# Kernel optimization log

Hardware: AMD Instinct MI355X
Metric: run time of the kernel (lower is better)

The kernel has to match this reference:

```python
import jax, jax.numpy as jnp
import numpy as np

B, S, E = 4, 2048, 1024
H = 4
DH = E // H          # 256 head dim
DQ = E // 4          # 256 quaternion d_model
ALPHA = 1.5
EPS = 1e-10
FOCUS = 0.9
SEL = 2.0


def setup_inputs() -> dict:
    key = jax.random.key(0)
    ks = jax.random.split(key, 6)
    sc = 0.02
    return {
        "x": jax.random.normal(ks[0], (B, S, E), dtype=jnp.float32),
        "in_proj_w": jax.random.normal(ks[1], (3 * E, E), dtype=jnp.float32) * sc,
        "in_proj_b": jnp.zeros((3 * E,), dtype=jnp.float32),
        "out_w": jax.random.normal(ks[2], (E, E), dtype=jnp.float32) * sc,
        "out_b": jnp.zeros((E,), dtype=jnp.float32),
        "m_w1": jax.random.normal(ks[3], (E, E), dtype=jnp.float32) * sc,
        "m_b1": jnp.zeros((E,), dtype=jnp.float32),
        "m_w2": jax.random.normal(ks[4], (E, E), dtype=jnp.float32) * sc,
        "m_b2": jnp.zeros((E,), dtype=jnp.float32),
    }


def quaternion_multiply(q1, q2):
    # Hamilton product over last dim of size 4 (complex-valued components).
    w1, x1, y1, z1 = q1[..., 0], q1[..., 1], q1[..., 2], q1[..., 3]
    w2, x2, y2, z2 = q2[..., 0], q2[..., 1], q2[..., 2], q2[..., 3]
    return jnp.stack([
        w1 * w2 - x1 * x2 - y1 * y2 - z1 * z2,
        w1 * x2 + x1 * w2 + y1 * z2 - z1 * y2,
        w1 * y2 - x1 * z2 + y1 * w2 + z1 * x2,
        w1 * z2 + x1 * y2 - y1 * x2 + z1 * w2,
    ], axis=-1)


def _mha(x, in_proj_w, in_proj_b, out_w, out_b):
    # torch nn.MultiheadAttention self-attention, batch_first
    qkv = x @ in_proj_w.T + in_proj_b              # [B,S,3E]
    q, k, v = jnp.split(qkv, 3, axis=-1)
    q = q.reshape(B, S, H, DH)
    k = k.reshape(B, S, H, DH)
    v = v.reshape(B, S, H, DH)
    scores = jnp.einsum('bqhd,bkhd->bhqk', q, k) / jnp.sqrt(jnp.float32(DH))
    attn = jax.nn.softmax(scores, axis=-1)
    out = jnp.einsum('bhqk,bkhd->bqhd', attn, v).reshape(B, S, E)
    return out @ out_w.T + out_b


def _spectral_attention(signal):
    sq = signal.reshape(B, S, DQ, 4)
    sfft = jnp.fft.fft(sq, axis=-3)                 # complex64, FFT over seq
    kk = jnp.arange(S, dtype=jnp.float32)
    filt = jnp.exp(1j * ALPHA * jnp.arctan(jnp.log(kk + EPS)))  # [S] complex
    sf = sfft * filt[None, :, None, None]
    inter = quaternion_multiply(quaternion_multiply(sf, sf), sf)
    attended = jnp.fft.ifft(inter, axis=-3).real
    return attended.reshape(B, S, E)


def reference(x, in_proj_w, in_proj_b, out_w, out_b, m_w1, m_b1, m_w2, m_b2):
    nicotinic = _mha(x, in_proj_w, in_proj_b, out_w, out_b)
    h = jax.nn.gelu(x @ m_w1.T + m_b1, approximate=False)
    muscarinic = h @ m_w2.T + m_b2
    chol = FOCUS * nicotinic + (1.0 - FOCUS) * muscarinic
    attn_w = _spectral_attention(chol * SEL)
    return x * attn_w
```

## Files before the change

### kernel.cpp

```cpp
#include <hip/hip_runtime.h>
#include <cstdint>

typedef _Float16 f16;
typedef unsigned short u16;
typedef __attribute__((ext_vector_type(8))) _Float16 half8;
typedef __attribute__((ext_vector_type(4))) _Float16 half4;
typedef __attribute__((ext_vector_type(2))) __fp16 fp16x2;
typedef __attribute__((ext_vector_type(4))) float f32x4;

#define MFMA_F16(a, b, c) __builtin_amdgcn_mfma_f32_16x16x32_f16(a, b, c, 0, 0, 0)

#define WAITVM8() asm volatile("s_waitcnt vmcnt(8)" ::: "memory")
#define WAITVM4() asm volatile("s_waitcnt vmcnt(4)" ::: "memory")
#define WAITVM2() asm volatile("s_waitcnt vmcnt(2)" ::: "memory")
#define WAITVM0() asm volatile("s_waitcnt vmcnt(0)" ::: "memory")
#define BARRIER() do { asm volatile("" ::: "memory"); __builtin_amdgcn_s_barrier(); \
                       asm volatile("" ::: "memory"); } while (0)

__device__ inline void stage16(const void* g, void* l) {
#if defined(__has_builtin) && __has_builtin(__builtin_amdgcn_global_load_lds)
  __builtin_amdgcn_global_load_lds(
      (const __attribute__((address_space(1))) unsigned*)g,
      (__attribute__((address_space(3))) unsigned*)l, 16, 0, 0);
#else
  *(int4*)l = *(const int4*)g;
#endif
}

__device__ inline int pack_f16(float a, float b) {
#if defined(__has_builtin) && __has_builtin(__builtin_amdgcn_cvt_pkrtz)
  union { fp16x2 h; int i; } u;
  u.h = __builtin_amdgcn_cvt_pkrtz(a, b);
  return u.i;
#else
  union { f16 h[2]; int i; } u;
  u.h[0] = (f16)a; u.h[1] = (f16)b;
  return u.i;
#endif
}

__global__ __launch_bounds__(256)
void conv_all(const float* __restrict__ x, const float* __restrict__ wqkv,
              const float* __restrict__ w1, const float* __restrict__ wout,
              const float* __restrict__ w2, f16* __restrict__ dst) {
  int i = (blockIdx.x * 256 + threadIdx.x) * 8;
  const float* src; size_t dofs; float sc = 1.0f;
  if (i < 8388608)       { src = x + i;               dofs = i; }
  else if (i < 11534336) { src = wqkv + (i - 8388608); dofs = i; }
  else if (i < 12582912) { src = w1 + (i - 11534336);  dofs = i; }
  else if (i < 13631488) {
    int t = i - 12582912; int j = t >> 10, k = t & 1023;
    src = wout + t; dofs = 12582912 + (size_t)j * 2048 + k; sc = 1.8f;
  } else {
    int t = i - 13631488; int j = t >> 10, k = t & 1023;
    src = w2 + t; dofs = 12582912 + (size_t)j * 2048 + 1024 + k; sc = 0.2f;
  }
  float4 a = *(const float4*)src;
  float4 b = *(const float4*)(src + 4);
  half8 h;
  h[0] = (f16)(a.x * sc); h[1] = (f16)(a.y * sc); h[2] = (f16)(a.z * sc); h[3] = (f16)(a.w * sc);
  h[4] = (f16)(b.x * sc); h[5] = (f16)(b.y * sc); h[6] = (f16)(b.z * sc); h[7] = (f16)(b.w * sc);
  *(half8*)(dst + dofs) = h;
}

template<int EPI>
__global__ __launch_bounds__(256, 2)
void gemm_f16(const f16* __restrict__ A, const f16* __restrict__ W,
              const float* __restrict__ bias0, const float* __restrict__ bias1,
              void* __restrict__ out0, void* __restrict__ out1,
              f16* __restrict__ Vt, int N, int K) {
  __shared__ __align__(16) f16 lds[2][16384];
  const int tid = threadIdx.x;
  const int lane = tid & 63, w = tid >> 6;
  const int g = lane >> 4, lm = lane & 15;
  const int wr = w >> 1, wc = w & 1;
  const int nwg = gridDim.x * gridDim.y;
  const int flat = blockIdx.y * gridDim.x + blockIdx.x;
  const int logical = (flat & 7) * (nwg >> 3) + (flat >> 3);
  const int bx = logical % gridDim.x, by = logical / gridDim.x;
  const int m0 = by * 128, n0 = bx * 128;

  const f16* src[8];
#pragma unroll
  for (int j = 0; j < 8; ++j) {
    int u = j * 256 + tid;
    if (u < 1024) {
      int row = u >> 3, s = u & 7;
      src[j] = A + (size_t)(m0 + row) * K + ((s ^ (row & 7)) << 3);
    } else {
      int v = u - 1024;
      int row = v >> 3, s = v & 7;
      src[j] = W + (size_t)(n0 + row) * K + ((s ^ (row & 7)) << 3);
    }
  }

  f32x4 acc[4][4];
#pragma unroll
  for (int mt = 0; mt < 4; ++mt)
#pragma unroll
    for (int nt = 0; nt < 4; ++nt) acc[mt][nt] = (f32x4){0.f, 0.f, 0.f, 0.f};

#pragma unroll
  for (int j = 0; j < 8; ++j) stage16(src[j], &lds[0][(j * 256 + tid) * 8]);
  __syncthreads();

  const int KT = K >> 6;
#pragma unroll 1
  for (int t = 0; t < KT; ++t) {
    const f16* bufA = lds[t & 1];
    const f16* bufB = bufA + 8192;
    if (t + 1 < KT) {
#pragma unroll
      for (int j = 0; j < 8; ++j) {
        src[j] += 64;
        stage16(src[j], &lds[(t + 1) & 1][(j * 256 + tid) * 8]);
      }
      WAITVM8();
    } else {
      WAITVM0();
    }
    BARRIER();
#pragma unroll
    for (int ks = 0; ks < 2; ++ks) {
      half8 a[4], b[4];
#pragma unroll
      for (int mt = 0; mt < 4; ++mt) {
        int row = wr * 64 + mt * 16 + lm;
        a[mt] = *(const half8*)(bufA + row * 64 + (((ks * 4 + g) ^ (row & 7)) << 3));
      }
#pragma unroll
      for (int nt = 0; nt < 4; ++nt) {
        int row = wc * 64 + nt * 16 + lm;
        b[nt] = *(const half8*)(bufB + row * 64 + (((ks * 4 + g) ^ (row & 7)) << 3));
      }
#pragma unroll
      for (int mt = 0; mt < 4; ++mt)
#pragma unroll
        for (int nt = 0; nt < 4; ++nt)
          acc[mt][nt] = MFMA_F16(a[mt], b[nt], acc[mt][nt]);
    }
    BARRIER();
  }

  const int crow = m0 + wr * 64 + g * 4;
  const int ccol = n0 + wc * 64 + lm;
  if (EPI == 3) {
    if (n0 < 2048) {
      f16* qk = (f16*)out0;
#pragma unroll
      for (int nt = 0; nt < 4; ++nt) {
        float bb = bias0[ccol + nt * 16];
#pragma unroll
        for (int mt = 0; mt < 4; ++mt)
#pragma unroll
          for (int r = 0; r < 4; ++r)
            qk[(size_t)(crow + mt * 16 + r) * 3072 + ccol + nt * 16] =
                (f16)(acc[mt][nt][r] + bb);
      }
    } else if (n0 < 3072) {
      f16* ldsT = (f16*)lds;
#pragma unroll
      for (int nt = 0; nt < 4; ++nt) {
        float bb = bias0[ccol + nt * 16];
        int c = wc * 64 + nt * 16 + lm;
#pragma unroll
        for (int mt = 0; mt < 4; ++mt) {
          int r = wr * 64 + mt * 16 + g * 4;
#pragma unroll
          for (int rr = 0; rr < 4; ++rr)
            ldsT[c * 136 + r + rr] = (f16)(acc[mt][nt][rr] + bb);
        }
      }
      BARRIER();
      const int vbase0 = n0 - 2048;
      const int b = m0 >> 11, srow = m0 & 2047;
#pragma unroll
      for (int it = 0; it < 8; ++it) {
        int id = it * 256 + tid;
        int c = id >> 4, rb = id & 15;
        int vcol = vbase0 + c;
        int h = vcol >> 8, d = vcol & 255;
        half8 v = *(half8*)&ldsT[c * 136 + rb * 8];
        *(half8*)&Vt[(((size_t)(b * 4 + h)) * 256 + d) * 2048 + srow + rb * 8] = v;
      }
    } else {
      f16* cat = (f16*)out1;
      const int hc = ccol - 3072;
#pragma unroll
      for (int nt = 0; nt < 4; ++nt) {
        float bb = bias1[hc + nt * 16];
#pragma unroll
        for (int mt = 0; mt < 4; ++mt)
#pragma unroll
          for (int r = 0; r < 4; ++r) {
            float v = acc[mt][nt][r] + bb;
            v = 0.5f * v * (1.0f + erff(v * 0.70710678118654752f));
            cat[(size_t)(crow + mt * 16 + r) * 2048 + 1024 + hc + nt * 16] = (f16)v;
          }
      }
    }
  } else {
    f16* ch = (f16*)out0;
#pragma unroll
    for (int nt = 0; nt < 4; ++nt) {
      float bb = 1.8f * bias0[ccol + nt * 16] + 0.2f * bias1[ccol + nt * 16];
#pragma unroll
      for (int mt = 0; mt < 4; ++mt)
#pragma unroll
        for (int r = 0; r < 4; ++r)
          ch[(size_t)(crow + mt * 16 + r) * 1024 + ccol + nt * 16] =
              (f16)(acc[mt][nt][r] + bb);
    }
  }
}

__global__ __launch_bounds__(512, 2)
void flash_f16(const f16* __restrict__ qkv, const f16* __restrict__ Vt,
               f16* __restrict__ attn) {
  __shared__ __align__(16) f16 lds[32768];
  const int tid = threadIdx.x;
  const int lane = tid & 63, w = tid >> 6;
  const int g = lane >> 4, lm = lane & 15;
  const int raw = blockIdx.x;
  const int bh = (raw & 7) * 2 + (raw >> 7);
  const int qt = (raw >> 3) & 15;
  const int b = bh >> 2, h = bh & 3;
  const int q0 = qt * 128 + w * 16;
  const float SC = 0.09016844005555896f;

  half8 qf[8];
  {
    const f16* qp = qkv + (size_t)(b * 2048 + q0 + lm) * 3072 + h * 256 + g * 8;
#pragma unroll
    for (int c = 0; c < 8; ++c) qf[c] = *(const half8*)(qp + c * 32);
  }

  const f16* kbase = qkv + (size_t)b * 2048 * 3072 + 1024 + h * 256;
  const f16* vbase = Vt + (size_t)bh * 256 * 2048;
  int kofs[2], vofs[2];
#pragma unroll
  for (int j = 0; j < 2; ++j) {
    int u = j * 512 + tid;
    int kv = u >> 5, s = u & 31;
    kofs[j] = kv * 3072 + ((s ^ (kv & 7)) << 3);
    int d = u >> 2, sl = u & 3;
    vofs[j] = d * 2048 + ((sl ^ ((d >> 1) & 3)) << 3);
  }

  f32x4 o[16];
#pragma unroll
  for (int f = 0; f < 16; ++f) o[f] = (f32x4){0.f, 0.f, 0.f, 0.f};
  float m = -3e38f, l = 0.f;
  half8 paP = (half8){0, 0, 0, 0, 0, 0, 0, 0};

#pragma unroll
  for (int j = 0; j < 2; ++j) stage16(kbase + kofs[j], &lds[(j * 512 + tid) * 8]);

#pragma unroll 1
  for (int t = 0; t < 64; ++t) {
    const int cb_ = t & 1;
    if (t < 63) {
      const int kt = (t + 1) * 98304;
#pragma unroll
      for (int j = 0; j < 2; ++j)
        stage16(kbase + kofs[j] + kt, &lds[(cb_ ^ 1) * 8192 + (j * 512 + tid) * 8]);
    }
    {
      const int vt_ = t * 32;
#pragma unroll
      for (int j = 0; j < 2; ++j)
        stage16(vbase + vofs[j] + vt_, &lds[16384 + cb_ * 8192 + (j * 512 + tid) * 8]);
    }
    if (t < 63) { WAITVM4(); } else { WAITVM2(); }
    BARRIER();

    const f16* kb = &lds[cb_ * 8192];

    f32x4 s0 = {0.f, 0.f, 0.f, 0.f}, s1 = {0.f, 0.f, 0.f, 0.f};
    __builtin_amdgcn_s_setprio(1);
#pragma unroll
    for (int c = 0; c < 8; ++c) {
      int slot = ((c * 4 + g) ^ (lm & 7)) << 3;
      half8 b0 = *(const half8*)(kb + lm * 256 + slot);
      half8 b1 = *(const half8*)(kb + (16 + lm) * 256 + slot);
      s0 = MFMA_F16(b0, qf[c], s0);
      s1 = MFMA_F16(b1, qf[c], s1);
    }
    __builtin_amdgcn_s_setprio(0);

    if (t > 0) {
      const f16* vbp = &lds[16384 + (cb_ ^ 1) * 8192];
      __builtin_amdgcn_s_setprio(1);
#pragma unroll
      for (int f = 0; f < 16; ++f) {
        int d = f * 16 + lm;
        half8 bv = *(const half8*)(vbp + d * 32 + ((g ^ ((d >> 1) & 3)) << 3));
        o[f] = MFMA_F16(paP, bv, o[f]);
      }
      __builtin_amdgcn_s_setprio(0);
    }

    float a0[4], a1[4];
#pragma unroll
    for (int r = 0; r < 4; ++r) { a0[r] = s0[r] * SC; a1[r] = s1[r] * SC; }
    float mx = fmaxf(fmaxf(fmaxf(a0[0], a0[1]), fmaxf(a0[2], a0[3])),
                     fmaxf(fmaxf(a1[0], a1[1]), fmaxf(a1[2], a1[3])));
    mx = fmaxf(mx, __shfl_xor(mx, 16));
    mx = fmaxf(mx, __shfl_xor(mx, 32));

    if (!__all(mx <= m + 8.0f)) {
      float mn = fmaxf(m, mx);
      float corr = exp2f(m - mn);
      m = mn; l *= corr;
#pragma unroll
      for (int r = 0; r < 4; ++r) {
        float cr = __shfl(corr, ((lane >> 2) & 12) + r);
#pragma unroll
        for (int f = 0; f < 16; ++f) o[f][r] *= cr;
      }
    }

    float e0[4], e1[4], rs;
#pragma unroll
    for (int r = 0; r < 4; ++r) { e0[r] = exp2f(a0[r] - m); e1[r] = exp2f(a1[r] - m); }
    rs = ((e0[0] + e0[1]) + (e0[2] + e0[3])) + ((e1[0] + e1[1]) + (e1[2] + e1[3]));
    rs += __shfl_xor(rs, 16);
    rs += __shfl_xor(rs, 32);
    l += rs;

    int A01 = pack_f16(e0[0], e0[1]);
    int A23 = pack_f16(e0[2], e0[3]);
    int B01 = pack_f16(e1[0], e1[1]);
    int B23 = pack_f16(e1[2], e1[3]);
    const int s1l = ((lane & 16) << 1) + lm;
    const int s2l = s1l + 16;
    int t0a = __shfl(A01, s1l), t0b = __shfl(B01, s1l);
    int t1a = __shfl(A23, s1l), t1b = __shfl(B23, s1l);
    int t2a = __shfl(A01, s2l), t2b = __shfl(B01, s2l);
    int t3a = __shfl(A23, s2l), t3b = __shfl(B23, s2l);
    union { int i[4]; half8 h; } pau;
    const bool hi = lane >= 32;
    pau.i[0] = hi ? t0b : t0a;
    pau.i[1] = hi ? t1b : t1a;
    pau.i[2] = hi ? t2b : t2a;
    pau.i[3] = hi ? t3b : t3a;
    paP = pau.h;

    BARRIER();
  }

  WAITVM0();
  BARRIER();
  {
    const f16* vbp = &lds[16384 + 8192];
#pragma unroll
    for (int f = 0; f < 16; ++f) {
      int d = f * 16 + lm;
      half8 bv = *(const half8*)(vbp + d * 32 + ((g ^ ((d >> 1) & 3)) << 3));
      o[f] = MFMA_F16(paP, bv, o[f]);
    }
  }

  float inv[4];
#pragma unroll
  for (int r = 0; r < 4; ++r) inv[r] = 1.0f / __shfl(l, ((lane >> 2) & 12) + r);
#pragma unroll
  for (int f = 0; f < 16; ++f)
#pragma unroll
    for (int r = 0; r < 4; ++r)
      attn[(size_t)(b * 2048 + q0 + g * 4 + r) * 2048 + h * 256 + f * 16 + lm] =
          (f16)(o[f][r] * inv[r]);
}

__device__ inline float2 cmul(float2 a, float2 b) {
  return make_float2(a.x * b.x - a.y * b.y, a.x * b.y + a.y * b.x);
}
__device__ inline float2 cmulc(float2 a, float2 b) {
  return make_float2(a.x * b.x + a.y * b.y, a.y * b.x - a.x * b.y);
}
__device__ inline void qcube(float2& w, float2& x, float2& y, float2& z, float2 f) {
  w = cmul(w, f); x = cmul(x, f); y = cmul(y, f); z = cmul(z, f);
  float2 a2 = cmul(w, w);
  float2 sx = cmul(x, x), sy = cmul(y, y), sz = cmul(z, z);
  float2 s = make_float2(sx.x + sy.x + sz.x, sx.y + sy.y + sz.y);
  float2 t3 = make_float2(a2.x - 3.f * s.x, a2.y - 3.f * s.y);
  float2 cf = make_float2(3.f * a2.x - s.x, 3.f * a2.y - s.y);
  w = cmul(w, t3); x = cmul(cf, x); y = cmul(cf, y); z = cmul(cf, z);
}

__device__ inline int fftpos(int k) {
  int kp = k >> 1;
  return ((k & 1) << 10) | ((kp & 3) << 8) | ((kp & 12) << 4) | (kp & 48)
       | ((kp >> 4) & 12) | ((kp >> 8) & 3);
}

__global__ __launch_bounds__(256)
void spectral4(const f16* __restrict__ chol, const float* __restrict__ xin,
               float* __restrict__ outp) {
  __shared__ __align__(16) float2 Z[2][2048];
  __shared__ float2 tw[1024];
  const int tid = threadIdx.x;
  const int b = blockIdx.x >> 8;
  const int qd = blockIdx.x & 255;
  const size_t c0 = (size_t)qd * 4;
  const f16* cb = chol + (size_t)b * 2048 * 1024;

  for (int j = tid; j < 1024; j += 256) {
    float ang = -6.2831853071795864769f * (float)j * (1.0f / 2048.0f);
    float sv, cv; sincosf(ang, &sv, &cv);
    tw[j] = make_float2(cv, sv);
  }
  for (int s = tid; s < 2048; s += 256) {
    half4 v = *(const half4*)(cb + (size_t)s * 1024 + c0);
    Z[0][s] = make_float2((float)v[0], (float)v[1]);
    Z[1][s] = make_float2((float)v[2], (float)v[3]);
  }
  __syncthreads();

#pragma unroll 1
  for (int it = 0; it < 8; ++it) {
    int gg = it * 256 + tid;
    int c = gg >> 10, j = gg & 1023;
    float2 a = Z[c][j], bb = Z[c][j + 1024];
    Z[c][j] = make_float2(a.x + bb.x, a.y + bb.y);
    Z[c][j + 1024] = cmul(make_float2(a.x - bb.x, a.y - bb.y), tw[j]);
  }
  __syncthreads();

#pragma unroll 1
  for (int lq = 8; lq >= 0; lq -= 2) {
    const int Q = 1 << lq, st = 512 >> lq;
#pragma unroll 1
    for (int it = 0; it < 4; ++it) {
      int gg = it * 256 + tid;
      int c = gg >> 9, bf = gg & 511;
      int j = bf & (Q - 1);
      int base = ((bf >> lq) << (lq + 2)) | j;
      float2 a = Z[c][base], bq = Z[c][base + Q];
      float2 cc = Z[c][base + 2 * Q], d = Z[c][base + 3 * Q];
      float2 t0 = make_float2(a.x + cc.x, a.y + cc.y);
      float2 t1 = make_float2(a.x - cc.x, a.y - cc.y);
      float2 t2 = make_float2(bq.x + d.x, bq.y + d.y);
      float2 bd = make_float2(bq.x - d.x, bq.y - d.y);
      float2 t3 = make_float2(bd.y, -bd.x);
      float2 y0 = make_float2(t0.x + t2.x, t0.y + t2.y);
      float2 y1 = make_float2(t1.x + t3.x, t1.y + t3.y);
      float2 y2 = make_float2(t0.x - t2.x, t0.y - t2.y);
      float2 y3 = make_float2(t1.x - t3.x, t1.y - t3.y);
      int i3 = 3 * j * st;
      float sg = (i3 & 1024) ? -1.f : 1.f;
      i3 &= 1023;
      Z[c][base] = y0;
      Z[c][base + Q] = cmul(y1, tw[j * st]);
      Z[c][base + 2 * Q] = cmul(y2, tw[2 * j * st]);
      float2 r3 = cmul(y3, tw[i3]);
      Z[c][base + 3 * Q] = make_float2(r3.x * sg, r3.y * sg);
    }
    __syncthreads();
  }

#pragma unroll 1
  for (int it = 0; it < 4; ++it) {
    int jj = it * 256 + tid;
    int nrep = (jj == 0) ? 2 : 1;
#pragma unroll 1
    for (int rep = 0; rep < nrep; ++rep) {
      int k  = (jj == 0) ? (rep ? 1024 : 0) : jj;
      int kn = (jj == 0) ? k : 2048 - jj;
      int p  = fftpos(k);
      int pp = fftpos(kn);
      float2 z0p = Z[0][p], z0q = Z[0][pp];
      float2 z1p = Z[1][p], z1q = Z[1][pp];
      float2 wk = make_float2(0.5f * (z0p.x + z0q.x), 0.5f * (z0p.y - z0q.y));
      float2 xk = make_float2(0.5f * (z0p.y + z0q.y), 0.5f * (z0q.x - z0p.x));
      float2 yk = make_float2(0.5f * (z1p.x + z1q.x), 0.5f * (z1p.y - z1q.y));
      float2 zk = make_float2(0.5f * (z1p.y + z1q.y), 0.5f * (z1q.x - z1p.x));
      float2 wn = make_float2(0.5f * (z0q.x + z0p.x), 0.5f * (z0q.y - z0p.y));
      float2 xn = make_float2(0.5f * (z0q.y + z0p.y), 0.5f * (z0p.x - z0q.x));
      float2 yn = make_float2(0.5f * (z1q.x + z1p.x), 0.5f * (z1q.y - z1p.y));
      float2 zn = make_float2(0.5f * (z1q.y + z1p.y), 0.5f * (z1p.x - z1q.x));
      float sk, ck, sn, cn;
      sincosf(1.5f * atanf(logf((float)k + 1e-10f)), &sk, &ck);
      sincosf(1.5f * atanf(logf((float)kn + 1e-10f)), &sn, &cn);
      qcube(wk, xk, yk, zk, make_float2(ck, sk));
      qcube(wn, xn, yn, zn, make_float2(cn, sn));
      Z[0][p]  = make_float2(0.5f * (wk.x + wn.x) - 0.5f * (xk.y - xn.y),
                             0.5f * (wk.y - wn.y) + 0.5f * (xk.x + xn.x));
      Z[0][pp] = make_float2(0.5f * (wn.x + wk.x) - 0.5f * (xn.y - xk.y),
                             0.5f * (wn.y - wk.y) + 0.5f * (xn.x + xk.x));
      Z[1][p]  = make_float2(0.5f * (yk.x + yn.x) - 0.5f * (zk.y - zn.y),
                             0.5f * (yk.y - yn.y) + 0.5f * (zk.x + zn.x));
      Z[1][pp] = make_float2(0.5f * (yn.x + yk.x) - 0.5f * (zn.y - zk.y),
                             0.5f * (yn.y - yk.y) + 0.5f * (zn.x + zk.x));
    }
  }
  __syncthreads();

#pragma unroll 1
  for (int lq = 0; lq <= 8; lq += 2) {
    const int Q = 1 << lq, st = 512 >> lq;
#pragma unroll 1
    for (int it = 0; it < 4; ++it) {
      int gg = it * 256 + tid;
      int c = gg >> 9, bf = gg & 511;
      int j = bf & (Q - 1);
      int base = ((bf >> lq) << (lq + 2)) | j;
      float2 a = Z[c][base];
      float2 bq = cmulc(Z[c][base + Q], tw[j * st]);
      float2 cc = cmulc(Z[c][base + 2 * Q], tw[2 * j * st]);
      int i3 = 3 * j * st;
      float sg = (i3 & 1024) ? -1.f : 1.f;
      i3 &= 1023;
      float2 d = cmulc(Z[c][base + 3 * Q], tw[i3]);
      d = make_float2(d.x * sg, d.y * sg);
      float2 t0 = make_float2(a.x + cc.x, a.y + cc.y);
      float2 t1 = make_float2(a.x - cc.x, a.y - cc.y);
      float2 t2 = make_float2(bq.x + d.x, bq.y + d.y);
      float2 bd = make_float2(bq.x - d.x, bq.y - d.y);
      float2 t3 = make_float2(-bd.y, bd.x);
      Z[c][base]         = make_float2(t0.x + t2.x, t0.y + t2.y);
      Z[c][base + Q]     = make_float2(t1.x + t3.x, t1.y + t3.y);
      Z[c][base + 2 * Q] = make_float2(t0.x - t2.x, t0.y - t2.y);
      Z[c][base + 3 * Q] = make_float2(t1.x - t3.x, t1.y - t3.y);
    }
    __syncthreads();
  }

#pragma unroll 1
  for (int it = 0; it < 8; ++it) {
    int gg = it * 256 + tid;
    int c = gg >> 10, j = gg & 1023;
    float2 a = Z[c][j];
    float2 bw = cmulc(Z[c][j + 1024], tw[j]);
    Z[c][j] = make_float2(a.x + bw.x, a.y + bw.y);
    Z[c][j + 1024] = make_float2(a.x - bw.x, a.y - bw.y);
  }
  __syncthreads();

  const float* xb = xin + (size_t)b * 2048 * 1024;
  float* ob = outp + (size_t)b * 2048 * 1024;
  const float inv = 1.0f / 2048.0f;
  for (int s = tid; s < 2048; s += 256) {
    float4 xv = *(const float4*)(xb + (size_t)s * 1024 + c0);
    float2 r0 = Z[0][s], r1 = Z[1][s];
    float4 o;
    o.x = xv.x * r0.x * inv;
    o.y = xv.y * r0.y * inv;
    o.z = xv.z * r1.x * inv;
    o.w = xv.w * r1.y * inv;
    *(float4*)(ob + (size_t)s * 1024 + c0) = o;
  }
}

extern "C" void kernel_launch(void* const* d_in, const int* in_sizes, int n_in,
                              void* d_out, int out_size, void* d_ws, size_t ws_size,
                              hipStream_t stream) {
  const float* x    = (const float*)d_in[0];
  const float* wqkv = (const float*)d_in[1];
  const float* bqkv = (const float*)d_in[2];
  const float* wout = (const float*)d_in[3];
  const float* bout = (const float*)d_in[4];
  const float* w1   = (const float*)d_in[5];
  const float* b1   = (const float*)d_in[6];
  const float* w2   = (const float*)d_in[7];
  const float* b2   = (const float*)d_in[8];
  float* out = (float*)d_out;
  char* wsb = (char*)d_ws;
  const size_t MB = 1048576;

  f16*   xf    = (f16*)(wsb);
  f16*   wqf   = (f16*)(wsb + 16 * MB);
  f16*   wcat  = (f16*)(wsb + 24 * MB);
  f16*   qkvF  = (f16*)(wsb + 32 * MB);
  f16*   VtF   = (f16*)(wsb + 80 * MB);
  f16*   cat   = (f16*)(wsb + 96 * MB);
  f16*   chol  = (f16*)(wsb + 128 * MB);

  conv_all<<<7168, 256, 0, stream>>>(x, wqkv, w1, wout, w2, xf);

  gemm_f16<3><<<dim3(32, 64), 256, 0, stream>>>(xf, wqf, bqkv, b1, qkvF, cat, VtF, 4096, 1024);
  flash_f16<<<256, 512, 0, stream>>>(qkvF, VtF, cat);
  gemm_f16<4><<<dim3(8, 64), 256, 0, stream>>>(cat, wcat, bout, b2, chol, nullptr, nullptr, 1024, 2048);
  spectral4<<<1024, 256, 0, stream>>>(chol, x, out);
}
```

Baseline: 360.6 us.

## Split flash attention over KV halves with combine kernel; precompute spectral filter table

Flash attention now runs with twice as many workgroups, each covering half of the key/value sequence. Each writes partial normalized outputs and per-row (max, sum) statistics, and a new combine kernel merges the two halves into the concatenated buffer. The goal is better GPU occupancy, since 256 workgroups underfill the device. The cost is an extra kernel launch and extra partial-output traffic. Separately, the per-frequency sincos/atan/log filter is precomputed once into a table instead of being evaluated inside the spectral kernel.

```diff
diff --git a/kernel.cpp b/kernel.cpp
--- a/kernel.cpp
+++ b/kernel.cpp
@@ -61,6 +61,16 @@
   h[0] = (f16)(a.x * sc); h[1] = (f16)(a.y * sc); h[2] = (f16)(a.z * sc); h[3] = (f16)(a.w * sc);
   h[4] = (f16)(b.x * sc); h[5] = (f16)(b.y * sc); h[6] = (f16)(b.z * sc); h[7] = (f16)(b.w * sc);
   *(half8*)(dst + dofs) = h;
+}
+
+__global__ __launch_bounds__(256)
+void filt_init(float2* __restrict__ ftab) {
+  int k = blockIdx.x * 256 + threadIdx.x;
+  if (k < 2048) {
+    float s, c;
+    sincosf(1.5f * atanf(logf((float)k + 1e-10f)), &s, &c);
+    ftab[k] = make_float2(c, s);
+  }
 }
 
 template<int EPI>
@@ -216,13 +226,14 @@
 
 __global__ __launch_bounds__(512, 2)
 void flash_f16(const f16* __restrict__ qkv, const f16* __restrict__ Vt,
-               f16* __restrict__ attn) {
+               f16* __restrict__ Op, float2* __restrict__ ML) {
   __shared__ __align__(16) f16 lds[32768];
   const int tid = threadIdx.x;
   const int lane = tid & 63, w = tid >> 6;
   const int g = lane >> 4, lm = lane & 15;
   const int raw = blockIdx.x;
-  const int bh = (raw & 7) * 2 + (raw >> 7);
+  const int kvh = raw >> 8;
+  const int bh = (raw & 7) * 2 + ((raw >> 7) & 1);
   const int qt = (raw >> 3) & 15;
   const int b = bh >> 2, h = bh & 3;
   const int q0 = qt * 128 + w * 16;
@@ -235,8 +246,9 @@
     for (int c = 0; c < 8; ++c) qf[c] = *(const half8*)(qp + c * 32);
   }
 
-  const f16* kbase = qkv + (size_t)b * 2048 * 3072 + 1024 + h * 256;
-  const f16* vbase = Vt + (size_t)bh * 256 * 2048;
+  const f16* kbase = qkv + (size_t)b * 2048 * 3072 + 1024 + h * 256
+                   + (size_t)kvh * 1024 * 3072;
+  const f16* vbase = Vt + (size_t)bh * 256 * 2048 + kvh * 1024;
   int kofs[2], vofs[2];
 #pragma unroll
   for (int j = 0; j < 2; ++j) {
@@ -257,9 +269,9 @@
   for (int j = 0; j < 2; ++j) stage16(kbase + kofs[j], &lds[(j * 512 + tid) * 8]);
 
 #pragma unroll 1
-  for (int t = 0; t < 64; ++t) {
+  for (int t = 0; t < 32; ++t) {
     const int cb_ = t & 1;
-    if (t < 63) {
+    if (t < 31) {
       const int kt = (t + 1) * 98304;
 #pragma unroll
       for (int j = 0; j < 2; ++j)
@@ -271,7 +283,7 @@
       for (int j = 0; j < 2; ++j)
         stage16(vbase + vofs[j] + vt_, &lds[16384 + cb_ * 8192 + (j * 512 + tid) * 8]);
     }
-    if (t < 63) { WAITVM4(); } else { WAITVM2(); }
+    if (t < 31) { WAITVM4(); } else { WAITVM2(); }
     BARRIER();
 
     const f16* kb = &lds[cb_ * 8192];
@@ -361,15 +373,42 @@
     }
   }
 
+  const size_t seg = (size_t)(kvh * 16 + bh) * 2048;
+  if (lane < 16) ML[seg + q0 + lm] = make_float2(m, l);
+
   float inv[4];
 #pragma unroll
   for (int r = 0; r < 4; ++r) inv[r] = 1.0f / __shfl(l, ((lane >> 2) & 12) + r);
+  f16* op = Op + (seg + q0) * 256;
 #pragma unroll
   for (int f = 0; f < 16; ++f)
 #pragma unroll
     for (int r = 0; r < 4; ++r)
-      attn[(size_t)(b * 2048 + q0 + g * 4 + r) * 2048 + h * 256 + f * 16 + lm] =
-          (f16)(o[f][r] * inv[r]);
+      op[(size_t)(g * 4 + r) * 256 + f * 16 + lm] = (f16)(o[f][r] * inv[r]);
+}
+
+__global__ __launch_bounds__(256)
+void combine(const f16* __restrict__ Op, const float2* __restrict__ ML,
+             f16* __restrict__ cat) {
+  int id = blockIdx.x * 256 + threadIdx.x;
+  int rrow = id >> 5;
+  int dseg = (id & 31) * 8;
+  int bh = rrow >> 11, q = rrow & 2047;
+  int b = bh >> 2, h = bh & 3;
+  float2 ml1 = ML[rrow];
+  float2 ml2 = ML[32768 + rrow];
+  float M = fmaxf(ml1.x, ml2.x);
+  float w1 = ml1.y * exp2f(ml1.x - M);
+  float w2 = ml2.y * exp2f(ml2.x - M);
+  float inv = 1.0f / (w1 + w2);
+  w1 *= inv; w2 *= inv;
+  half8 o1 = *(const half8*)(Op + (size_t)rrow * 256 + dseg);
+  half8 o2 = *(const half8*)(Op + (size_t)(32768 + rrow) * 256 + dseg);
+  half8 out;
+#pragma unroll
+  for (int j = 0; j < 8; ++j)
+    out[j] = (f16)((float)o1[j] * w1 + (float)o2[j] * w2);
+  *(half8*)(cat + ((size_t)(b * 2048 + q)) * 2048 + h * 256 + dseg) = out;
 }
 
 __device__ inline float2 cmul(float2 a, float2 b) {
@@ -395,8 +434,8 @@
 }
 
 __global__ __launch_bounds__(256)
-void spectral4(const f16* __restrict__ chol, const float* __restrict__ xin,
-               float* __restrict__ outp) {
+void spectral5(const f16* __restrict__ chol, const float* __restrict__ xin,
+               const float2* __restrict__ ftab, float* __restrict__ outp) {
   __shared__ __align__(16) float2 Z[2][2048];
   __shared__ float2 tw[1024];
   const int tid = threadIdx.x;
@@ -479,11 +518,9 @@
       float2 xn = make_float2(0.5f * (z0q.y + z0p.y), 0.5f * (z0p.x - z0q.x));
       float2 yn = make_float2(0.5f * (z1q.x + z1p.x), 0.5f * (z1q.y - z1p.y));
       float2 zn = make_float2(0.5f * (z1q.y + z1p.y), 0.5f * (z1p.x - z1q.x));
-      float sk, ck, sn, cn;
-      sincosf(1.5f * atanf(logf((float)k + 1e-10f)), &sk, &ck);
-      sincosf(1.5f * atanf(logf((float)kn + 1e-10f)), &sn, &cn);
-      qcube(wk, xk, yk, zk, make_float2(ck, sk));
-      qcube(wn, xn, yn, zn, make_float2(cn, sn));
+      float2 fk = ftab[k], fn = ftab[kn];
+      qcube(wk, xk, yk, zk, fk);
+      qcube(wn, xn, yn, zn, fn);
       Z[0][p]  = make_float2(0.5f * (wk.x + wn.x) - 0.5f * (xk.y - xn.y),
                              0.5f * (wk.y - wn.y) + 0.5f * (xk.x + xn.x));
       Z[0][pp] = make_float2(0.5f * (wn.x + wk.x) - 0.5f * (xn.y - xk.y),
@@ -575,11 +612,16 @@
   f16*   VtF   = (f16*)(wsb + 80 * MB);
   f16*   cat   = (f16*)(wsb + 96 * MB);
   f16*   chol  = (f16*)(wsb + 128 * MB);
-
+  f16*   Op    = (f16*)(wsb + 144 * MB);
+  float2* ML   = (float2*)(wsb + 178 * MB);
+  float2* ftab = (float2*)(wsb + 179 * MB);
+
+  filt_init<<<8, 256, 0, stream>>>(ftab);
   conv_all<<<7168, 256, 0, stream>>>(x, wqkv, w1, wout, w2, xf);
 
   gemm_f16<3><<<dim3(32, 64), 256, 0, stream>>>(xf, wqf, bqkv, b1, qkvF, cat, VtF, 4096, 1024);
-  flash_f16<<<256, 512, 0, stream>>>(qkvF, VtF, cat);
+  flash_f16<<<512, 512, 0, stream>>>(qkvF, VtF, Op, ML);
+  combine<<<4096, 256, 0, stream>>>(Op, ML, cat);
   gemm_f16<4><<<dim3(8, 64), 256, 0, stream>>>(cat, wcat, bout, b2, chol, nullptr, nullptr, 1024, 2048);
-  spectral4<<<1024, 256, 0, stream>>>(chol, x, out);
-}
+  spectral5<<<1024, 256, 0, stream>>>(chol, x, ftab, out);
+}
```

Measured after the change: 382.2 us. 6.0% more time.

## Transpose chol output via LDS, fuse first/last FFT stages, precompute filter table

Applied to the files above, without the earlier changes.

The combine GEMM epilogue now stages its tile through LDS and writes chol transposed (channel-major), so each spectral block reads contiguous sequence runs per channel. The spectral kernel folds the first radix-2 FFT stage into the load loop and the final inverse radix-2 stage into the output loop, which removes two LDS passes and two barriers. The per-frequency filter (log/atan/sincos) is computed once by a small init kernel into a table instead of inside every block. This adds an extra kernel launch, an LDS barrier in the GEMM epilogue, and scalar f16 global loads in the spectral kernel.

```diff
diff --git a/kernel.cpp b/kernel.cpp
--- a/kernel.cpp
+++ b/kernel.cpp
@@ -61,6 +61,16 @@
   h[0] = (f16)(a.x * sc); h[1] = (f16)(a.y * sc); h[2] = (f16)(a.z * sc); h[3] = (f16)(a.w * sc);
   h[4] = (f16)(b.x * sc); h[5] = (f16)(b.y * sc); h[6] = (f16)(b.z * sc); h[7] = (f16)(b.w * sc);
   *(half8*)(dst + dofs) = h;
+}
+
+__global__ __launch_bounds__(256)
+void filt_init(float2* __restrict__ ftab) {
+  int k = blockIdx.x * 256 + threadIdx.x;
+  if (k < 2048) {
+    float s, c;
+    sincosf(1.5f * atanf(logf((float)k + 1e-10f)), &s, &c);
+    ftab[k] = make_float2(c, s);
+  }
 }
 
 template<int EPI>
@@ -200,16 +210,27 @@
       }
     }
   } else {
-    f16* ch = (f16*)out0;
+    f16* ldsT = (f16*)lds;
 #pragma unroll
     for (int nt = 0; nt < 4; ++nt) {
       float bb = 1.8f * bias0[ccol + nt * 16] + 0.2f * bias1[ccol + nt * 16];
-#pragma unroll
-      for (int mt = 0; mt < 4; ++mt)
-#pragma unroll
-        for (int r = 0; r < 4; ++r)
-          ch[(size_t)(crow + mt * 16 + r) * 1024 + ccol + nt * 16] =
-              (f16)(acc[mt][nt][r] + bb);
+      int c = wc * 64 + nt * 16 + lm;
+#pragma unroll
+      for (int mt = 0; mt < 4; ++mt) {
+        int r = wr * 64 + mt * 16 + g * 4;
+#pragma unroll
+        for (int rr = 0; rr < 4; ++rr)
+          ldsT[c * 136 + r + rr] = (f16)(acc[mt][nt][rr] + bb);
+      }
+    }
+    BARRIER();
+    f16* ch = (f16*)out0;
+#pragma unroll
+    for (int it = 0; it < 8; ++it) {
+      int id = it * 256 + tid;
+      int c = id >> 4, rb = id & 15;
+      half8 v = *(half8*)&ldsT[c * 136 + rb * 8];
+      *(half8*)&ch[(size_t)(n0 + c) * 8192 + m0 + rb * 8] = v;
     }
   }
 }
@@ -395,35 +416,34 @@
 }
 
 __global__ __launch_bounds__(256)
-void spectral4(const f16* __restrict__ chol, const float* __restrict__ xin,
-               float* __restrict__ outp) {
+void spectral6(const f16* __restrict__ cholT, const float* __restrict__ xin,
+               const float2* __restrict__ ftab, float* __restrict__ outp) {
   __shared__ __align__(16) float2 Z[2][2048];
   __shared__ float2 tw[1024];
   const int tid = threadIdx.x;
   const int b = blockIdx.x >> 8;
   const int qd = blockIdx.x & 255;
   const size_t c0 = (size_t)qd * 4;
-  const f16* cb = chol + (size_t)b * 2048 * 1024;
+  const f16* t0 = cholT + (c0 + 0) * 8192 + b * 2048;
+  const f16* t1 = cholT + (c0 + 1) * 8192 + b * 2048;
+  const f16* t2 = cholT + (c0 + 2) * 8192 + b * 2048;
+  const f16* t3 = cholT + (c0 + 3) * 8192 + b * 2048;
 
   for (int j = tid; j < 1024; j += 256) {
     float ang = -6.2831853071795864769f * (float)j * (1.0f / 2048.0f);
     float sv, cv; sincosf(ang, &sv, &cv);
     tw[j] = make_float2(cv, sv);
   }
-  for (int s = tid; s < 2048; s += 256) {
-    half4 v = *(const half4*)(cb + (size_t)s * 1024 + c0);
-    Z[0][s] = make_float2((float)v[0], (float)v[1]);
-    Z[1][s] = make_float2((float)v[2], (float)v[3]);
-  }
-  __syncthreads();
-
-#pragma unroll 1
-  for (int it = 0; it < 8; ++it) {
-    int gg = it * 256 + tid;
-    int c = gg >> 10, j = gg & 1023;
-    float2 a = Z[c][j], bb = Z[c][j + 1024];
-    Z[c][j] = make_float2(a.x + bb.x, a.y + bb.y);
-    Z[c][j + 1024] = cmul(make_float2(a.x - bb.x, a.y - bb.y), tw[j]);
+  for (int s = tid; s < 1024; s += 256) {
+    float2 z0a = make_float2((float)t0[s], (float)t1[s]);
+    float2 z1a = make_float2((float)t2[s], (float)t3[s]);
+    float2 z0b = make_float2((float)t0[s + 1024], (float)t1[s + 1024]);
+    float2 z1b = make_float2((float)t2[s + 1024], (float)t3[s + 1024]);
+    float2 w = tw[s];
+    Z[0][s] = make_float2(z0a.x + z0b.x, z0a.y + z0b.y);
+    Z[0][s + 1024] = cmul(make_float2(z0a.x - z0b.x, z0a.y - z0b.y), w);
+    Z[1][s] = make_float2(z1a.x + z1b.x, z1a.y + z1b.y);
+    Z[1][s + 1024] = cmul(make_float2(z1a.x - z1b.x, z1a.y - z1b.y), w);
   }
   __syncthreads();
 
@@ -438,15 +458,15 @@
       int base = ((bf >> lq) << (lq + 2)) | j;
       float2 a = Z[c][base], bq = Z[c][base + Q];
       float2 cc = Z[c][base + 2 * Q], d = Z[c][base + 3 * Q];
-      float2 t0 = make_float2(a.x + cc.x, a.y + cc.y);
-      float2 t1 = make_float2(a.x - cc.x, a.y - cc.y);
-      float2 t2 = make_float2(bq.x + d.x, bq.y + d.y);
+      float2 t0_ = make_float2(a.x + cc.x, a.y + cc.y);
+      float2 t1_ = make_float2(a.x - cc.x, a.y - cc.y);
+      float2 t2_ = make_float2(bq.x + d.x, bq.y + d.y);
       float2 bd = make_float2(bq.x - d.x, bq.y - d.y);
-      float2 t3 = make_float2(bd.y, -bd.x);
-      float2 y0 = make_float2(t0.x + t2.x, t0.y + t2.y);
-      float2 y1 = make_float2(t1.x + t3.x, t1.y + t3.y);
-      float2 y2 = make_float2(t0.x - t2.x, t0.y - t2.y);
-      float2 y3 = make_float2(t1.x - t3.x, t1.y - t3.y);
+      float2 t3_ = make_float2(bd.y, -bd.x);
+      float2 y0 = make_float2(t0_.x + t2_.x, t0_.y + t2_.y);
+      float2 y1 = make_float2(t1_.x + t3_.x, t1_.y + t3_.y);
+      float2 y2 = make_float2(t0_.x - t2_.x, t0_.y - t2_.y);
+      float2 y3 = make_float2(t1_.x - t3_.x, t1_.y - t3_.y);
       int i3 = 3 * j * st;
       float sg = (i3 & 1024) ? -1.f : 1.f;
       i3 &= 1023;
@@ -479,11 +499,9 @@
       float2 xn = make_float2(0.5f * (z0q.y + z0p.y), 0.5f * (z0p.x - z0q.x));
       float2 yn = make_float2(0.5f * (z1q.x + z1p.x), 0.5f * (z1q.y - z1p.y));
       float2 zn = make_float2(0.5f * (z1q.y + z1p.y), 0.5f * (z1p.x - z1q.x));
-      float sk, ck, sn, cn;
-      sincosf(1.5f * atanf(logf((float)k + 1e-10f)), &sk, &ck);
-      sincosf(1.5f * atanf(logf((float)kn + 1e-10f)), &sn, &cn);
-      qcube(wk, xk, yk, zk, make_float2(ck, sk));
-      qcube(wn, xn, yn, zn, make_float2(cn, sn));
+      float2 fk = ftab[k], fn = ftab[kn];
+      qcube(wk, xk, yk, zk, fk);
+      qcube(wn, xn, yn, zn, fn);
       Z[0][p]  = make_float2(0.5f * (wk.x + wn.x) - 0.5f * (xk.y - xn.y),
                              0.5f * (wk.y - wn.y) + 0.5f * (xk.x + xn.x));
       Z[0][pp] = make_float2(0.5f * (wn.x + wk.x) - 0.5f * (xn.y - xk.y),
@@ -513,42 +531,43 @@
       i3 &= 1023;
       float2 d = cmulc(Z[c][base + 3 * Q], tw[i3]);
       d = make_float2(d.x * sg, d.y * sg);
-      float2 t0 = make_float2(a.x + cc.x, a.y + cc.y);
-      float2 t1 = make_float2(a.x - cc.x, a.y - cc.y);
-      float2 t2 = make_float2(bq.x + d.x, bq.y + d.y);
+      float2 t0_ = make_float2(a.x + cc.x, a.y + cc.y);
+      float2 t1_ = make_float2(a.x - cc.x, a.y - cc.y);
+      float2 t2_ = make_float2(bq.x + d.x, bq.y + d.y);
       float2 bd = make_float2(bq.x - d.x, bq.y - d.y);
-      float2 t3 = make_float2(-bd.y, bd.x);
-      Z[c][base]         = make_float2(t0.x + t2.x, t0.y + t2.y);
-      Z[c][base + Q]     = make_float2(t1.x + t3.x, t1.y + t3.y);
-      Z[c][base + 2 * Q] = make_float2(t0.x - t2.x, t0.y - t2.y);
-      Z[c][base + 3 * Q] = make_float2(t1.x - t3.x, t1.y - t3.y);
+      float2 t3_ = make_float2(-bd.y, bd.x);
+      Z[c][base]         = make_float2(t0_.x + t2_.x, t0_.y + t2_.y);
+      Z[c][base + Q]     = make_float2(t1_.x + t3_.x, t1_.y + t3_.y);
+      Z[c][base + 2 * Q] = make_float2(t0_.x - t2_.x, t0_.y - t2_.y);
+      Z[c][base + 3 * Q] = make_float2(t1_.x - t3_.x, t1_.y - t3_.y);
     }
     __syncthreads();
   }
-
-#pragma unroll 1
-  for (int it = 0; it < 8; ++it) {
-    int gg = it * 256 + tid;
-    int c = gg >> 10, j = gg & 1023;
-    float2 a = Z[c][j];
-    float2 bw = cmulc(Z[c][j + 1024], tw[j]);
-    Z[c][j] = make_float2(a.x + bw.x, a.y + bw.y);
-    Z[c][j + 1024] = make_float2(a.x - bw.x, a.y - bw.y);
-  }
-  __syncthreads();
 
   const float* xb = xin + (size_t)b * 2048 * 1024;
   float* ob = outp + (size_t)b * 2048 * 1024;
   const float inv = 1.0f / 2048.0f;
-  for (int s = tid; s < 2048; s += 256) {
-    float4 xv = *(const float4*)(xb + (size_t)s * 1024 + c0);
-    float2 r0 = Z[0][s], r1 = Z[1][s];
-    float4 o;
-    o.x = xv.x * r0.x * inv;
-    o.y = xv.y * r0.y * inv;
-    o.z = xv.z * r1.x * inv;
-    o.w = xv.w * r1.y * inv;
-    *(float4*)(ob + (size_t)s * 1024 + c0) = o;
+  for (int j = tid; j < 1024; j += 256) {
+    float2 wj = tw[j];
+    float2 a0 = Z[0][j], bw0 = cmulc(Z[0][j + 1024], wj);
+    float2 a1 = Z[1][j], bw1 = cmulc(Z[1][j + 1024], wj);
+    float2 r0lo = make_float2(a0.x + bw0.x, a0.y + bw0.y);
+    float2 r0hi = make_float2(a0.x - bw0.x, a0.y - bw0.y);
+    float2 r1lo = make_float2(a1.x + bw1.x, a1.y + bw1.y);
+    float2 r1hi = make_float2(a1.x - bw1.x, a1.y - bw1.y);
+    float4 xlo = *(const float4*)(xb + (size_t)j * 1024 + c0);
+    float4 xhi = *(const float4*)(xb + (size_t)(j + 1024) * 1024 + c0);
+    float4 olo, ohi;
+    olo.x = xlo.x * r0lo.x * inv;
+    olo.y = xlo.y * r0lo.y * inv;
+    olo.z = xlo.z * r1lo.x * inv;
+    olo.w = xlo.w * r1lo.y * inv;
+    ohi.x = xhi.x * r0hi.x * inv;
+    ohi.y = xhi.y * r0hi.y * inv;
+    ohi.z = xhi.z * r1hi.x * inv;
+    ohi.w = xhi.w * r1hi.y * inv;
+    *(float4*)(ob + (size_t)j * 1024 + c0) = olo;
+    *(float4*)(ob + (size_t)(j + 1024) * 1024 + c0) = ohi;
   }
 }
 
@@ -574,12 +593,14 @@
   f16*   qkvF  = (f16*)(wsb + 32 * MB);
   f16*   VtF   = (f16*)(wsb + 80 * MB);
   f16*   cat   = (f16*)(wsb + 96 * MB);
-  f16*   chol  = (f16*)(wsb + 128 * MB);
-
+  f16*   cholT = (f16*)(wsb + 128 * MB);
+  float2* ftab = (float2*)(wsb + 145 * MB);
+
+  filt_init<<<8, 256, 0, stream>>>(ftab);
   conv_all<<<7168, 256, 0, stream>>>(x, wqkv, w1, wout, w2, xf);
 
   gemm_f16<3><<<dim3(32, 64), 256, 0, stream>>>(xf, wqf, bqkv, b1, qkvF, cat, VtF, 4096, 1024);
   flash_f16<<<256, 512, 0, stream>>>(qkvF, VtF, cat);
-  gemm_f16<4><<<dim3(8, 64), 256, 0, stream>>>(cat, wcat, bout, b2, chol, nullptr, nullptr, 1024, 2048);
-  spectral4<<<1024, 256, 0, stream>>>(chol, x, out);
-}
+  gemm_f16<4><<<dim3(8, 64), 256, 0, stream>>>(cat, wcat, bout, b2, cholT, nullptr, nullptr, 1024, 2048);
+  spectral6<<<1024, 256, 0, stream>>>(cholT, x, ftab, out);
+}
```

After: 352.7 us. -2.2%, faster.
